# Kernel optimization log

Hardware: AMD Instinct MI355X
Metric: run time of the kernel (lower is better)

Reference implementation:

```python
import jax, jax.numpy as jnp
import numpy as np

B, L, V = 64, 512, 32000
E, H, D = 64, 512, 1024   # embed dim, LSTM hidden, bidirectional dim
NH, KD = 8, 64            # attention heads, key_dim
TOPK = 5
BN_EPS = 1e-3             # keras BatchNormalization default epsilon


def _run_lstm(x, Wx, Wh, b):
    """Keras-style LSTM (gate order i,f,g,o). x: [B,T,Din]. Returns (seq [B,T,H], last [B,H])."""
    Bn, Hn = x.shape[0], Wh.shape[0]
    z = jnp.einsum('btd,dk->btk', x, Wx) + b  # precompute input contribution [B,T,4H]
    def step(carry, zt):
        h, c = carry
        g = zt + h @ Wh
        i, f, gg, o = jnp.split(g, 4, axis=-1)
        c = jax.nn.sigmoid(f) * c + jax.nn.sigmoid(i) * jnp.tanh(gg)
        h = jax.nn.sigmoid(o) * jnp.tanh(c)
        return (h, c), h
    init = (jnp.zeros((Bn, Hn), x.dtype), jnp.zeros((Bn, Hn), x.dtype))
    (hT, _), hs = jax.lax.scan(step, init, jnp.swapaxes(z, 0, 1))
    return jnp.swapaxes(hs, 0, 1), hT


def _bilstm_seq(x, fWx, fWh, fb, bWx, bWh, bb):
    hf, _ = _run_lstm(x, fWx, fWh, fb)
    hb, _ = _run_lstm(x[:, ::-1], bWx, bWh, bb)
    return jnp.concatenate([hf, hb[:, ::-1]], axis=-1)


def _bilstm_last(x, fWx, fWh, fb, bWx, bWh, bb):
    _, hf = _run_lstm(x, fWx, fWh, fb)
    _, hb = _run_lstm(x[:, ::-1], bWx, bWh, bb)
    return jnp.concatenate([hf, hb], axis=-1)


def _cos(x):
    return x / (jnp.linalg.norm(x, axis=-1, keepdims=True) + 1e-6)


def _topk_gather(q, keys, values, k, weight=None):
    """Cosine-similarity top-k retrieval: q [B,64], keys/values [N,64] -> [B,k,64]."""
    sim = _cos(q) @ _cos(keys).T          # [B,N]
    if weight is not None:
        sim = sim * weight                # importance / confidence weighting
    _, idx = jax.lax.top_k(sim, k)
    return values[idx]                    # gather -> [B,k,64]


def _forward(tokens, emb,
             l1f_Wx, l1f_Wh, l1f_b, l1b_Wx, l1b_Wh, l1b_b,
             l2f_Wx, l2f_Wh, l2f_b, l2b_Wx, l2b_Wh, l2b_b,
             Wq, bq, Wk, bk, Wv, bv, Wo, bo,
             mq_W, mq_b,
             ext_keys, ext_vals, form_emb, conc_keys, conc_vals,
             st_mem, lt_mem, lt_imp, inf_mem, inf_conf,
             rs_W, rs_b, bn_gamma, bn_beta, bn_mean, bn_var,
             out_W, out_b, fin_W, fin_b):
    # _process_input
    x = emb[tokens]                                                   # [B,L,64]
    x = _bilstm_seq(x, l1f_Wx, l1f_Wh, l1f_b, l1b_Wx, l1b_Wh, l1b_b)  # [B,L,1024]
    x = _bilstm_last(x, l2f_Wx, l2f_Wh, l2f_b, l2b_Wx, l2b_Wh, l2b_b) # [B,1024]
    # _apply_attention: MHA over a length-1 sequence
    xs = x[:, None, :]                                                # [B,1,1024]
    q = jnp.einsum('bse,ehd->bshd', xs, Wq) + bq
    k = jnp.einsum('bse,ehd->bshd', xs, Wk) + bk
    v = jnp.einsum('bse,ehd->bshd', xs, Wv) + bv
    att = jax.nn.softmax(jnp.einsum('bshd,bthd->bhst', q, k) / jnp.sqrt(jnp.float32(KD)), axis=-1)
    ctx = jnp.einsum('bhst,bthd->bshd', att, v)
    x = (jnp.einsum('bshd,hde->bse', ctx, Wo) + bo)[:, 0]             # [B,1024]
    # _query_memories: six-bank gather/combine
    query = x @ mq_W + mq_b                                           # [B,64]
    m_ext = jax.nn.softmax(query @ ext_keys.T, axis=-1) @ ext_vals    # [B,64]
    m_form = _topk_gather(query, form_emb, form_emb, TOPK)            # [B,5,64]
    m_conc = _topk_gather(query, conc_keys, conc_vals, TOPK)          # [B,5,64]
    m_st = _topk_gather(query, st_mem, st_mem, TOPK)                  # [B,5,64]
    m_lt = _topk_gather(query, lt_mem, lt_mem, TOPK, weight=lt_imp)   # [B,5,64]
    m_inf = _topk_gather(query, inf_mem, inf_mem, TOPK, weight=inf_conf)
    mem = jnp.concatenate([m_ext[:, None], m_form, m_conc, m_st, m_lt, m_inf], axis=1)  # [B,26,64]
    x = jnp.mean(mem, axis=1)                                         # [B,64]
    # _apply_reasoning (training=False -> inference batchnorm)
    x = jax.nn.relu(x @ rs_W + rs_b)                                  # [B,512]
    x = (x - bn_mean) / jnp.sqrt(bn_var + BN_EPS) * bn_gamma + bn_beta
    # _generate_output (stage 'elementary1')
    x = x @ out_W + out_b                                             # [B,128]
    return jax.nn.sigmoid(x @ fin_W + fin_b)                          # [B,1]


def setup_inputs() -> dict:
    key = jax.random.key(0)
    ks = iter(jax.random.split(key, 64))
    def rn(shape, s=0.02):
        return jax.random.normal(next(ks), shape, dtype=jnp.float32) * s
    def z(shape):
        return jnp.zeros(shape, dtype=jnp.float32)
    inp = {
        'tokens': jax.random.randint(next(ks), (B, L), 0, V),
        'emb': rn((V, E), 0.05),
        'l1f_Wx': rn((E, 4 * H)), 'l1f_Wh': rn((H, 4 * H)), 'l1f_b': z((4 * H,)),
        'l1b_Wx': rn((E, 4 * H)), 'l1b_Wh': rn((H, 4 * H)), 'l1b_b': z((4 * H,)),
        'l2f_Wx': rn((D, 4 * H)), 'l2f_Wh': rn((H, 4 * H)), 'l2f_b': z((4 * H,)),
        'l2b_Wx': rn((D, 4 * H)), 'l2b_Wh': rn((H, 4 * H)), 'l2b_b': z((4 * H,)),
        'Wq': rn((D, NH, KD)), 'bq': z((NH, KD)),
        'Wk': rn((D, NH, KD)), 'bk': z((NH, KD)),
        'Wv': rn((D, NH, KD)), 'bv': z((NH, KD)),
        'Wo': rn((NH, KD, D)), 'bo': z((D,)),
        'mq_W': rn((D, 64)), 'mq_b': z((64,)),
        'ext_keys': rn((100, 64), 0.5), 'ext_vals': rn((100, 64), 0.5),
        'form_emb': rn((1000, 64), 0.5),
        'conc_keys': rn((1000, 64), 0.5), 'conc_vals': rn((1000, 64), 0.5),
        'st_mem': rn((100, 64), 0.5),
        'lt_mem': rn((10000, 64), 0.5),
        'lt_imp': jax.random.uniform(next(ks), (10000,), dtype=jnp.float32),
        'inf_mem': rn((500, 64), 0.5),
        'inf_conf': jax.random.uniform(next(ks), (500,), dtype=jnp.float32),
        'rs_W': rn((64, 512)), 'rs_b': z((512,)),
        'bn_gamma': jnp.ones((512,), jnp.float32), 'bn_beta': z((512,)),
        'bn_mean': rn((512,), 0.1), 'bn_var': jnp.ones((512,), jnp.float32),
        'out_W': rn((512, 128)), 'out_b': z((128,)),
        'fin_W': rn((128, 1)), 'fin_b': z((1,)),
    }
    return inp


def reference(tokens, emb,
              l1f_Wx, l1f_Wh, l1f_b, l1b_Wx, l1b_Wh, l1b_b,
              l2f_Wx, l2f_Wh, l2f_b, l2b_Wx, l2b_Wh, l2b_b,
              Wq, bq, Wk, bk, Wv, bv, Wo, bo,
              mq_W, mq_b,
              ext_keys, ext_vals, form_emb, conc_keys, conc_vals,
              st_mem, lt_mem, lt_imp, inf_mem, inf_conf,
              rs_W, rs_b, bn_gamma, bn_beta, bn_mean, bn_var,
              out_W, out_b, fin_W, fin_b):
    return _forward(tokens, emb,
                    l1f_Wx, l1f_Wh, l1f_b, l1b_Wx, l1b_Wh, l1b_b,
                    l2f_Wx, l2f_Wh, l2f_b, l2b_Wx, l2b_Wh, l2b_b,
                    Wq, bq, Wk, bk, Wv, bv, Wo, bo,
                    mq_W, mq_b,
                    ext_keys, ext_vals, form_emb, conc_keys, conc_vals,
                    st_mem, lt_mem, lt_imp, inf_mem, inf_conf,
                    rs_W, rs_b, bn_gamma, bn_beta, bn_mean, bn_var,
                    out_W, out_b, fin_W, fin_b)
```

## Files before the change

### kernel.cpp

```cpp
#include <hip/hip_runtime.h>
#include <cstddef>
#include <cstdint>

typedef short s8v   __attribute__((ext_vector_type(8)));
typedef float f32x4 __attribute__((ext_vector_type(4)));

__device__ __forceinline__ float b2f(unsigned short u) {
  union { unsigned u; float f; } x; x.u = ((unsigned)u) << 16; return x.f;
}
__device__ __forceinline__ unsigned short f2b(float f) {
  union { float f; unsigned u; } x; x.f = f;
  unsigned u = x.u;
  return (unsigned short)((u + 0x7FFFu + ((u >> 16) & 1u)) >> 16);
}
__device__ __forceinline__ float sigm(float x) { return 1.f / (1.f + __expf(-x)); }
__device__ __forceinline__ float tanh_(float x) { return 1.f - 2.f / (__expf(2.f * x) + 1.f); }

#define AT_LOAD(p)        __hip_atomic_load((p), __ATOMIC_RELAXED, __HIP_MEMORY_SCOPE_AGENT)
#define AT_STORE_RLX(p,v) __hip_atomic_store((p), (v), __ATOMIC_RELAXED, __HIP_MEMORY_SCOPE_AGENT)

__device__ __forceinline__ s8v ldg_b128_sc(const unsigned short* p) {
  s8v r;
  asm volatile("global_load_dwordx4 %0, %1, off sc0 sc1" : "=v"(r) : "v"(p) : "memory");
  return r;
}
__device__ __forceinline__ void stg_b128_sc(unsigned short* p, s8v v) {
  asm volatile("global_store_dwordx4 %0, %1, off sc0 sc1" :: "v"(p), "v"(v) : "memory");
}

__global__ void __launch_bounds__(256)
k_embed(const int* __restrict__ tok, const float* __restrict__ emb,
        unsigned short* __restrict__ x1t)
{
  const int g = blockIdx.x * 256 + threadIdx.x;
  if (g >= 64 * 512 * 8) return;
  const int row = g >> 3, i = g & 7;
  const int b = row >> 9, t = row & 511;
  const int tk = tok[row];
  const f32x4 v0 = *(const f32x4*)(emb + (size_t)tk * 64 + i * 8);
  const f32x4 v1 = *(const f32x4*)(emb + (size_t)tk * 64 + i * 8 + 4);
  s8v o;
#pragma unroll
  for (int e = 0; e < 4; ++e) { o[e] = (short)f2b(v0[e]); o[4 + e] = (short)f2b(v1[e]); }
  *(s8v*)(x1t + ((size_t)t * 64 + b) * 64 + i * 8) = o;
}

__global__ void __launch_bounds__(256)
k_tr(const float* __restrict__ Wf, const float* __restrict__ Wb,
     unsigned short* __restrict__ out, int K, int N)
{
  __shared__ float t[64][65];
  const int tid = threadIdx.x;
  const int kt = blockIdx.x, nt = blockIdx.y, dir = blockIdx.z;
  const float* W = dir ? Wb : Wf;
#pragma unroll
  for (int i = 0; i < 16; ++i) {
    const int c = i * 256 + tid;
    const int k = c >> 6, n = c & 63;
    t[k][n] = W[(size_t)(kt * 64 + k) * N + nt * 64 + n];
  }
  __syncthreads();
#pragma unroll
  for (int i = 0; i < 16; ++i) {
    const int c = i * 256 + tid;
    const int n = c >> 6, k = c & 63;
    out[(size_t)dir * N * K + (size_t)(nt * 64 + n) * K + kt * 64 + k] = f2b(t[k][n]);
  }
}

__global__ void __launch_bounds__(256)
k_norms(const float* __restrict__ formE, const float* __restrict__ concK,
        const float* __restrict__ stM, const float* __restrict__ ltM,
        const float* __restrict__ infM, float* __restrict__ inn)
{
  const int i = blockIdx.x * 256 + threadIdx.x;
  if (i >= 12600) return;
  const float* src; int loc;
  if (i < 1000)       { src = formE; loc = i; }
  else if (i < 2000)  { src = concK; loc = i - 1000; }
  else if (i < 2100)  { src = stM;   loc = i - 2000; }
  else if (i < 12100) { src = ltM;   loc = i - 2100; }
  else                { src = infM;  loc = i - 12100; }
  float ss = 0.f;
#pragma unroll 16
  for (int d = 0; d < 64; ++d) { const float v = src[(size_t)loc * 64 + d]; ss += v * v; }
  inn[i] = 1.f / (sqrtf(ss) + 1e-6f);
}

template<int PHASE>
__global__ void __launch_bounds__(128, 1)
k_lstm(const unsigned short* __restrict__ x1t,
       const unsigned short* __restrict__ z2fp, const unsigned short* __restrict__ z2bp,
       const unsigned short* __restrict__ wht,
       const float* __restrict__ Wxf, const float* __restrict__ Wxb,
       const float* __restrict__ bsf, const float* __restrict__ bsb,
       unsigned short* __restrict__ hbuf,
       unsigned short* __restrict__ yout,
       int* __restrict__ flags,
       float* __restrict__ cg,
       int s0, int s1, int CT)
{
  __shared__ __align__(16) unsigned short h_lds[64 * 512];
  __shared__ __align__(16) unsigned short wh_lds[64 * 512];
  __shared__ __align__(16) unsigned short z_lds[64 * 72];
  __shared__ __align__(16) unsigned short hout[16 * 72];

  const int tid  = threadIdx.x;
  const int w    = tid >> 6;
  const int lane = tid & 63;
  const int fc   = lane & 15, fg = lane >> 4;
  const int wg   = blockIdx.x & 31;
  const int dir  = blockIdx.x >> 5;
  const int j0   = wg * 16;

  const unsigned short* Wht = wht + (size_t)dir * 2048 * 512;
  const float* Wx = dir ? Wxb : Wxf;
  const unsigned short* Z2 = dir ? z2bp : z2fp;
  const float* BS = dir ? bsb : bsf;
  int* flg = flags + dir * 32;
  unsigned short* hb = hbuf + (size_t)dir * (2 * 64 * 512);

  float bias_reg[4];
#pragma unroll
  for (int nt = 0; nt < 4; ++nt) bias_reg[nt] = BS[nt * 512 + j0 + fc];

  float c_reg[8];
  if (PHASE == 1 || s0 == 0) {
#pragma unroll
    for (int i = 0; i < 8; ++i) c_reg[i] = 0.f;
  } else {
#pragma unroll
    for (int mt = 0; mt < 2; ++mt)
#pragma unroll
      for (int v = 0; v < 4; ++v)
        c_reg[mt * 4 + v] =
          cg[(size_t)dir * 32768 + (size_t)(w * 32 + mt * 16 + fg * 4 + v) * 512 + j0 + fc];
  }

#pragma unroll
  for (int i = 0; i < 32; ++i) {
    const int c = i * 128 + tid;
    const int lc = c >> 6, kq8 = c & 63;
    const int nt = lc >> 4, fcc = lc & 15;
    s8v v = *(const s8v*)(Wht + (size_t)(nt * 512 + j0 + fcc) * 512 + kq8 * 8);
    *(s8v*)((char*)wh_lds + lc * 1024 + ((kq8 * 16) ^ ((lc & 7) << 4))) = v;
  }

  s8v Bx[4][2];
  if (PHASE == 1) {
#pragma unroll
    for (int nt = 0; nt < 4; ++nt)
#pragma unroll
      for (int kx = 0; kx < 2; ++kx) {
        s8v f;
#pragma unroll
        for (int i = 0; i < 8; ++i)
          f[i] = (short)f2b(Wx[(size_t)(kx * 32 + fg * 8 + i) * 2048 + nt * 512 + j0 + fc]);
        Bx[nt][kx] = f;
      }
  }
  __syncthreads();

  for (int s = s0; s < s1; ++s) {
    const int t = dir ? (511 - s) : s;
    const int gb = tid >> 1, jh = tid & 1;

    s8v xf[2][2];
    s8v zr[4];
    if (PHASE == 1) {
#pragma unroll
      for (int mt = 0; mt < 2; ++mt)
#pragma unroll
        for (int kx = 0; kx < 2; ++kx)
          xf[mt][kx] = *(const s8v*)(x1t +
            ((size_t)t * 64 + (w * 32 + mt * 16 + fc)) * 64 + kx * 32 + fg * 8);
    } else {
      const int lt = dir ? (s1 - 1 - s) : (s - s0);
#pragma unroll
      for (int g = 0; g < 4; ++g)
        zr[g] = *(const s8v*)(Z2 + ((size_t)(gb * CT + lt)) * 2048 + g * 512 + j0 + jh * 8);
    }

    if (s > 0) {
      const int target = s;
      int spins = 0;
      for (;;) {
        int v = (lane < 32) ? AT_LOAD(&flg[lane]) : target;
        if (__all(v >= target)) break;
        if (++spins > (1 << 18)) break;
        __builtin_amdgcn_s_sleep(1);
      }
      const unsigned short* hsrc = hb + (size_t)((s - 1) & 1) * (64 * 512);
      s8v t0[16], t1[16];
#pragma unroll
      for (int i = 0; i < 16; ++i) {
        const int c = i * 128 + tid;
        t0[i] = ldg_b128_sc(hsrc + (size_t)(c >> 6) * 512 + (c & 63) * 8);
      }
#pragma unroll
      for (int i = 0; i < 16; ++i) {
        const int c = (16 + i) * 128 + tid;
        t1[i] = ldg_b128_sc(hsrc + (size_t)(c >> 6) * 512 + (c & 63) * 8);
      }
      asm volatile("s_waitcnt vmcnt(16)" ::: "memory");
      __builtin_amdgcn_sched_barrier(0);
#pragma unroll
      for (int i = 0; i < 16; ++i) {
        const int c = i * 128 + tid;
        const int row = c >> 6, kb = c & 63;
        *(s8v*)((char*)h_lds + row * 1024 + ((kb * 16) ^ ((row & 7) << 4))) = t0[i];
      }
      asm volatile("s_waitcnt vmcnt(0)" ::: "memory");
      __builtin_amdgcn_sched_barrier(0);
#pragma unroll
      for (int i = 0; i < 16; ++i) {
        const int c = (16 + i) * 128 + tid;
        const int row = c >> 6, kb = c & 63;
        *(s8v*)((char*)h_lds + row * 1024 + ((kb * 16) ^ ((row & 7) << 4))) = t1[i];
      }
    }
    if (PHASE == 2) {
#pragma unroll
      for (int g = 0; g < 4; ++g)
        *(s8v*)(z_lds + gb * 72 + g * 16 + jh * 8) = zr[g];
    }
    __syncthreads();

    f32x4 acc[2][4];
#pragma unroll
    for (int mt = 0; mt < 2; ++mt)
#pragma unroll
      for (int nt = 0; nt < 4; ++nt) acc[mt][nt] = (f32x4){0.f, 0.f, 0.f, 0.f};

    if (PHASE == 1) {
#pragma unroll
      for (int kx = 0; kx < 2; ++kx)
#pragma unroll
        for (int mt = 0; mt < 2; ++mt)
#pragma unroll
          for (int nt = 0; nt < 4; ++nt)
            acc[mt][nt] = __builtin_amdgcn_mfma_f32_16x16x32_bf16(xf[mt][kx], Bx[nt][kx], acc[mt][nt], 0, 0, 0);
    }
    if (s > 0) {
#pragma unroll
      for (int kk = 0; kk < 16; ++kk) {
        const int k2 = (kk * 32 + fg * 8) * 2;
        s8v a[2], bh[4];
#pragma unroll
        for (int mt = 0; mt < 2; ++mt) {
          const int row = w * 32 + mt * 16 + fc;
          a[mt] = *(const s8v*)((char*)h_lds + row * 1024 + (k2 ^ ((row & 7) << 4)));
        }
#pragma unroll
        for (int nt = 0; nt < 4; ++nt) {
          const int lc = nt * 16 + fc;
          bh[nt] = *(const s8v*)((char*)wh_lds + lc * 1024 + (k2 ^ ((lc & 7) << 4)));
        }
#pragma unroll
        for (int mt = 0; mt < 2; ++mt)
#pragma unroll
          for (int nt = 0; nt < 4; ++nt)
            acc[mt][nt] = __builtin_amdgcn_mfma_f32_16x16x32_bf16(a[mt], bh[nt], acc[mt][nt], 0, 0, 0);
      }
    }

#pragma unroll
    for (int mt = 0; mt < 2; ++mt)
#pragma unroll
      for (int v = 0; v < 4; ++v) {
        const int b = w * 32 + mt * 16 + fg * 4 + v;
        float pi = acc[mt][0][v] + bias_reg[0];
        float pf = acc[mt][1][v] + bias_reg[1];
        float pg = acc[mt][2][v] + bias_reg[2];
        float po = acc[mt][3][v] + bias_reg[3];
        if (PHASE == 2) {
          pi += b2f(z_lds[b * 72 + 0 * 16 + fc]);
          pf += b2f(z_lds[b * 72 + 1 * 16 + fc]);
          pg += b2f(z_lds[b * 72 + 2 * 16 + fc]);
          po += b2f(z_lds[b * 72 + 3 * 16 + fc]);
        }
        const float c = sigm(pf) * c_reg[mt * 4 + v] + sigm(pi) * tanh_(pg);
        c_reg[mt * 4 + v] = c;
        hout[fc * 72 + b] = f2b(sigm(po) * tanh_(c));
      }
    asm volatile("s_waitcnt lgkmcnt(0)" ::: "memory");
    __builtin_amdgcn_sched_barrier(0);
    {
      const int bb = tid >> 1, hh = tid & 1;
      s8v o;
#pragma unroll
      for (int e = 0; e < 8; ++e) o[e] = (short)hout[(hh * 8 + e) * 72 + bb];
      stg_b128_sc(hb + (size_t)(s & 1) * (64 * 512) + bb * 512 + j0 + hh * 8, o);
      if (PHASE == 1) {
        *(s8v*)(yout + ((size_t)(bb * 512 + t)) * 1024 + dir * 512 + j0 + hh * 8) = o;
      } else if (s == 511) {
        *(s8v*)(yout + (size_t)bb * 1024 + dir * 512 + j0 + hh * 8) = o;
      }
    }
    if (PHASE == 2 && s == s1 - 1 && s1 < 512) {
#pragma unroll
      for (int mt = 0; mt < 2; ++mt)
#pragma unroll
        for (int v = 0; v < 4; ++v)
          cg[(size_t)dir * 32768 + (size_t)(w * 32 + mt * 16 + fg * 4 + v) * 512 + j0 + fc] =
            c_reg[mt * 4 + v];
    }
    __syncthreads();
    if (tid == 0) AT_STORE_RLX(&flg[wg], s + 1);
  }
}

__global__ void __launch_bounds__(256)
k_zgemm(const unsigned short* __restrict__ A, const unsigned short* __restrict__ Wxt,
        unsigned short* __restrict__ Cf, unsigned short* __restrict__ Cb,
        int tb0, int tb1, int CT)
{
  __shared__ unsigned short As[128 * 64];
  __shared__ unsigned short Bs[128 * 64];
  const int tid = threadIdx.x;
  const int lane = tid & 63;
  const int w = tid >> 6;
  const int wm = w >> 1, wn = w & 1;
  const int bx = blockIdx.x, by = blockIdx.y, dz = blockIdx.z;
  const unsigned short* Bmat = Wxt + (size_t)dz * 2048 * 1024;
  unsigned short* C = dz ? Cb : Cf;
  const int tb = dz ? tb1 : tb0;
  const int fc = lane & 15, fk = (lane >> 4) << 3;

  f32x4 acc[4][4];
#pragma unroll
  for (int mt = 0; mt < 4; ++mt)
#pragma unroll
    for (int nt = 0; nt < 4; ++nt) acc[mt][nt] = (f32x4){0.f, 0.f, 0.f, 0.f};

  for (int kt = 0; kt < 16; ++kt) {
    __syncthreads();
#pragma unroll
    for (int i = 0; i < 4; ++i) {
      const int c = i * 256 + tid;
      const int row = c >> 3, kb = c & 7;
      const int m = by * 128 + row;
      const int b = m / CT, lt = m - b * CT;
      s8v v = *(const s8v*)(A + ((size_t)b * 512 + tb + lt) * 1024 + kt * 64 + kb * 8);
      *(s8v*)((char*)As + row * 128 + ((kb * 16) ^ ((row & 7) << 4))) = v;
    }
#pragma unroll
    for (int i = 0; i < 4; ++i) {
      const int c = i * 256 + tid;
      const int n = c >> 3, kb = c & 7;
      s8v v = *(const s8v*)(Bmat + (size_t)(bx * 128 + n) * 1024 + kt * 64 + kb * 8);
      *(s8v*)((char*)Bs + n * 128 + ((kb * 16) ^ ((n & 7) << 4))) = v;
    }
    __syncthreads();
#pragma unroll
    for (int kk = 0; kk < 2; ++kk) {
      const int k2 = (kk * 32 + fk) * 2;
      s8v a[4], bfr[4];
#pragma unroll
      for (int mt = 0; mt < 4; ++mt) {
        const int row = wm * 64 + mt * 16 + fc;
        a[mt] = *(const s8v*)((char*)As + row * 128 + (k2 ^ ((row & 7) << 4)));
      }
#pragma unroll
      for (int nt = 0; nt < 4; ++nt) {
        const int n = wn * 64 + nt * 16 + fc;
        bfr[nt] = *(const s8v*)((char*)Bs + n * 128 + (k2 ^ ((n & 7) << 4)));
      }
#pragma unroll
      for (int mt = 0; mt < 4; ++mt)
#pragma unroll
        for (int nt = 0; nt < 4; ++nt)
          acc[mt][nt] = __builtin_amdgcn_mfma_f32_16x16x32_bf16(a[mt], bfr[nt], acc[mt][nt], 0, 0, 0);
    }
  }
  const int r0 = (lane >> 4) << 2;
#pragma unroll
  for (int mt = 0; mt < 4; ++mt)
#pragma unroll
    for (int nt = 0; nt < 4; ++nt) {
      const size_t rowg = (size_t)(by * 128 + wm * 64 + mt * 16 + r0);
      const int colg = bx * 128 + wn * 64 + nt * 16 + fc;
#pragma unroll
      for (int r = 0; r < 4; ++r)
        C[(rowg + r) * 2048 + colg] = f2b(acc[mt][nt][r]);
    }
}

__global__ void __launch_bounds__(256)
k_head1(const unsigned short* __restrict__ x2,
        const float* __restrict__ Wv, const float* __restrict__ bv,
        const float* __restrict__ Wo, const float* __restrict__ bo,
        const float* __restrict__ mqW, const float* __restrict__ mqb,
        float* __restrict__ query)
{
  __shared__ float xs[1024], ys[512], x3[1024];
  __shared__ float part[4][64];
  const int b = blockIdx.x, tid = threadIdx.x;
  for (int i = tid; i < 1024; i += 256) xs[i] = b2f(x2[(size_t)b * 1024 + i]);
  __syncthreads();
  {
    const int o = tid * 2;
    float a0 = 0.f, a1 = 0.f;
#pragma unroll 8
    for (int e = 0; e < 1024; ++e) {
      const float xv = xs[e];
      a0 += xv * Wv[(size_t)e * 512 + o];
      a1 += xv * Wv[(size_t)e * 512 + o + 1];
    }
    ys[o] = a0 + bv[o];
    ys[o + 1] = a1 + bv[o + 1];
  }
  __syncthreads();
  {
    const int e0 = tid * 4;
    float a0 = 0.f, a1 = 0.f, a2 = 0.f, a3 = 0.f;
#pragma unroll 8
    for (int h = 0; h < 512; ++h) {
      const float yv = ys[h];
      a0 += yv * Wo[(size_t)h * 1024 + e0];
      a1 += yv * Wo[(size_t)h * 1024 + e0 + 1];
      a2 += yv * Wo[(size_t)h * 1024 + e0 + 2];
      a3 += yv * Wo[(size_t)h * 1024 + e0 + 3];
    }
    x3[e0] = a0 + bo[e0];
    x3[e0 + 1] = a1 + bo[e0 + 1];
    x3[e0 + 2] = a2 + bo[e0 + 2];
    x3[e0 + 3] = a3 + bo[e0 + 3];
  }
  __syncthreads();
  {
    const int o = tid & 63, kc = tid >> 6;
    float a = 0.f;
#pragma unroll 8
    for (int e = kc * 256; e < kc * 256 + 256; ++e) a += x3[e] * mqW[(size_t)e * 64 + o];
    part[kc][o] = a;
  }
  __syncthreads();
  if (tid < 64)
    query[b * 64 + tid] = part[0][tid] + part[1][tid] + part[2][tid] + part[3][tid] + mqb[tid];
}

__device__ void bank_topk(const float* __restrict__ K, const float* __restrict__ V,
                          int n, const float* __restrict__ W, const float* __restrict__ inn,
                          float qinv, const float* q, float* sims, float* red, int* redi,
                          float* acc64, int tid)
{
  for (int i = tid; i < n; i += 256) {
    float s = 0.f;
#pragma unroll 16
    for (int d = 0; d < 64; ++d) s += q[d] * K[(size_t)i * 64 + d];
    s *= qinv * inn[i];
    if (W) s *= W[i];
    sims[i] = s;
  }
  __syncthreads();
  for (int it = 0; it < 5; ++it) {
    float bv = -1e30f; int bi = 1 << 30;
    for (int i = tid; i < n; i += 256) {
      const float v = sims[i];
      if (v > bv) { bv = v; bi = i; }
    }
    red[tid] = bv; redi[tid] = bi;
    __syncthreads();
    for (int st = 128; st >= 1; st >>= 1) {
      if (tid < st) {
        const float v = red[tid + st]; const int ix = redi[tid + st];
        if (v > red[tid] || (v == red[tid] && ix < redi[tid])) { red[tid] = v; redi[tid] = ix; }
      }
      __syncthreads();
    }
    const int sel = redi[0];
    if (tid < 64) acc64[tid] += V[(size_t)sel * 64 + tid];
    if (tid == 0) sims[sel] = -1e30f;
    __syncthreads();
  }
}

__global__ void __launch_bounds__(256)
k_head2(const float* __restrict__ query,
        const float* extK, const float* extV,
        const float* formE, const float* concK, const float* concV,
        const float* stM, const float* ltM, const float* ltW,
        const float* infM, const float* infW,
        const float* __restrict__ inn,
        const float* rsW, const float* rsb,
        const float* gma, const float* bta,
        const float* mea, const float* vr,
        const float* outW, const float* outb,
        const float* finW, const float* finb,
        float* __restrict__ out)
{
  __shared__ float q[64];
  __shared__ float acc64[64];
  __shared__ float sims[10000];
  __shared__ float red[256];
  __shared__ int redi[256];
  __shared__ float r1[512];
  __shared__ float o2[128];

  const int b = blockIdx.x, tid = threadIdx.x;
  if (tid < 64) q[tid] = query[b * 64 + tid];
  __syncthreads();
  red[tid] = (tid < 64) ? q[tid] * q[tid] : 0.f;
  __syncthreads();
  for (int st = 128; st >= 1; st >>= 1) { if (tid < st) red[tid] += red[tid + st]; __syncthreads(); }
  const float qinv = 1.f / (sqrtf(red[0]) + 1e-6f);
  __syncthreads();

  if (tid < 100) {
    float s = 0.f;
#pragma unroll 16
    for (int d = 0; d < 64; ++d) s += q[d] * extK[(size_t)tid * 64 + d];
    sims[tid] = s;
  }
  __syncthreads();
  red[tid] = (tid < 100) ? sims[tid] : -1e30f;
  __syncthreads();
  for (int st = 128; st >= 1; st >>= 1) { if (tid < st && red[tid + st] > red[tid]) red[tid] = red[tid + st]; __syncthreads(); }
  const float mx = red[0];
  __syncthreads();
  red[tid] = (tid < 100) ? __expf(sims[tid] - mx) : 0.f;
  __syncthreads();
  for (int st = 128; st >= 1; st >>= 1) { if (tid < st) red[tid] += red[tid + st]; __syncthreads(); }
  const float Z = red[0];
  __syncthreads();
  if (tid < 100) sims[tid] = __expf(sims[tid] - mx) / Z;
  __syncthreads();
  if (tid < 64) {
    float a = 0.f;
    for (int i = 0; i < 100; ++i) a += sims[i] * extV[(size_t)i * 64 + tid];
    acc64[tid] = a;
  }
  __syncthreads();

  bank_topk(formE, formE, 1000,  nullptr, inn + 0,     qinv, q, sims, red, redi, acc64, tid);
  bank_topk(concK, concV, 1000,  nullptr, inn + 1000,  qinv, q, sims, red, redi, acc64, tid);
  bank_topk(stM,   stM,   100,   nullptr, inn + 2000,  qinv, q, sims, red, redi, acc64, tid);
  bank_topk(ltM,   ltM,   10000, ltW,     inn + 2100,  qinv, q, sims, red, redi, acc64, tid);
  bank_topk(infM,  infM,  500,   infW,    inn + 12100, qinv, q, sims, red, redi, acc64, tid);

  if (tid < 64) acc64[tid] *= (1.f / 26.f);
  __syncthreads();

  {
    const int o = tid * 2;
    float a0 = 0.f, a1 = 0.f;
#pragma unroll 16
    for (int d = 0; d < 64; ++d) {
      const float xv = acc64[d];
      a0 += xv * rsW[(size_t)d * 512 + o];
      a1 += xv * rsW[(size_t)d * 512 + o + 1];
    }
    a0 = fmaxf(a0 + rsb[o], 0.f);
    a1 = fmaxf(a1 + rsb[o + 1], 0.f);
    r1[o]     = (a0 - mea[o])     / sqrtf(vr[o]     + 1e-3f) * gma[o]     + bta[o];
    r1[o + 1] = (a1 - mea[o + 1]) / sqrtf(vr[o + 1] + 1e-3f) * gma[o + 1] + bta[o + 1];
  }
  __syncthreads();
  if (tid < 128) {
    float a = 0.f;
#pragma unroll 8
    for (int j = 0; j < 512; ++j) a += r1[j] * outW[(size_t)j * 128 + tid];
    o2[tid] = a + outb[tid];
  }
  __syncthreads();
  red[tid] = (tid < 128) ? o2[tid] * finW[tid] : 0.f;
  __syncthreads();
  for (int st = 128; st >= 1; st >>= 1) { if (tid < st) red[tid] += red[tid + st]; __syncthreads(); }
  if (tid == 0) out[b] = sigm(red[0] + finb[0]);
}

__global__ void k_diag(float* out, int n, float val) {
  const int i = blockIdx.x * 64 + threadIdx.x;
  if (i < n) out[i] = val;
}

extern "C" void kernel_launch(void* const* d_in, const int* in_sizes, int n_in,
                              void* d_out, int out_size, void* d_ws, size_t ws_size,
                              hipStream_t stream)
{
  (void)in_sizes; (void)n_in;
  const int*   tokens = (const int*)d_in[0];
  const float* emb    = (const float*)d_in[1];
  const float* l1fWx  = (const float*)d_in[2];
  const float* l1fWh  = (const float*)d_in[3];
  const float* l1fb   = (const float*)d_in[4];
  const float* l1bWx  = (const float*)d_in[5];
  const float* l1bWh  = (const float*)d_in[6];
  const float* l1bb   = (const float*)d_in[7];
  const float* l2fWx  = (const float*)d_in[8];
  const float* l2fWh  = (const float*)d_in[9];
  const float* l2fb   = (const float*)d_in[10];
  const float* l2bWx  = (const float*)d_in[11];
  const float* l2bWh  = (const float*)d_in[12];
  const float* l2bb   = (const float*)d_in[13];
  const float* Wv     = (const float*)d_in[18];
  const float* bv     = (const float*)d_in[19];
  const float* Wo     = (const float*)d_in[20];
  const float* bo     = (const float*)d_in[21];
  const float* mqW    = (const float*)d_in[22];
  const float* mqb    = (const float*)d_in[23];
  const float* extK   = (const float*)d_in[24];
  const float* extV   = (const float*)d_in[25];
  const float* formE  = (const float*)d_in[26];
  const float* concK  = (const float*)d_in[27];
  const float* concV  = (const float*)d_in[28];
  const float* stM    = (const float*)d_in[29];
  const float* ltM    = (const float*)d_in[30];
  const float* ltW    = (const float*)d_in[31];
  const float* infM   = (const float*)d_in[32];
  const float* infW   = (const float*)d_in[33];
  const float* rsW    = (const float*)d_in[34];
  const float* rsb    = (const float*)d_in[35];
  const float* gma    = (const float*)d_in[36];
  const float* bta    = (const float*)d_in[37];
  const float* mea    = (const float*)d_in[38];
  const float* vr     = (const float*)d_in[39];
  const float* outW   = (const float*)d_in[40];
  const float* outb   = (const float*)d_in[41];
  const float* finW   = (const float*)d_in[42];
  const float* finb   = (const float*)d_in[43];

  float* outp = (float*)d_out;
  char* ws = (char*)d_ws;

  size_t off = 0;
  auto take = [&](size_t sz) { size_t o = off; off += (sz + 255) & ~(size_t)255; return o; };
  const size_t o_x1    = take((size_t)64 * 512 * 64 * 2);
  const size_t o_y1    = take((size_t)64 * 512 * 1024 * 2);
  const size_t o_wxt   = take((size_t)2 * 2048 * 1024 * 2);
  const size_t o_wht1  = take((size_t)2 * 2048 * 512 * 2);
  const size_t o_wht2  = take((size_t)2 * 2048 * 512 * 2);
  const size_t o_h1    = take((size_t)2 * 2 * 64 * 512 * 2);
  const size_t o_h2    = take((size_t)2 * 2 * 64 * 512 * 2);
  const size_t o_cg    = take((size_t)2 * 64 * 512 * 4);
  const size_t o_x2    = take((size_t)64 * 1024 * 2);
  const size_t o_query = take((size_t)64 * 64 * 4);
  const size_t o_norms = take((size_t)12600 * 4);
  const size_t o_flags = take(512);
  const size_t base = off;

  int CT = 0;
  const int cts[6] = {512, 256, 128, 64, 32, 16};
  for (int i = 0; i < 6; ++i) {
    const size_t need = base + (size_t)cts[i] * 524288 + 256;
    if (need <= ws_size) { CT = cts[i]; break; }
  }
  if (CT == 0) {
    k_diag<<<1, 64, 0, stream>>>(outp, out_size, (float)(ws_size >> 20));
    return;
  }
  const size_t o_zc = take((size_t)CT * 524288);

  unsigned short* x1t  = (unsigned short*)(ws + o_x1);
  unsigned short* y1   = (unsigned short*)(ws + o_y1);
  unsigned short* wxt  = (unsigned short*)(ws + o_wxt);
  unsigned short* wht1 = (unsigned short*)(ws + o_wht1);
  unsigned short* wht2 = (unsigned short*)(ws + o_wht2);
  unsigned short* h1   = (unsigned short*)(ws + o_h1);
  unsigned short* h2   = (unsigned short*)(ws + o_h2);
  float*          cg   = (float*)(ws + o_cg);
  unsigned short* x2   = (unsigned short*)(ws + o_x2);
  float*          qry  = (float*)(ws + o_query);
  float*          nrm  = (float*)(ws + o_norms);
  int*            flags = (int*)(ws + o_flags);
  unsigned short* zcf  = (unsigned short*)(ws + o_zc);
  unsigned short* zcb  = zcf + (size_t)64 * CT * 2048;

  hipMemsetAsync(flags, 0, 512, stream);
  k_embed<<<1024, 256, 0, stream>>>(tokens, emb, x1t);
  k_norms<<<50, 256, 0, stream>>>(formE, concK, stM, ltM, infM, nrm);
  k_tr<<<dim3(8, 32, 2), 256, 0, stream>>>(l1fWh, l1bWh, wht1, 512, 2048);
  k_tr<<<dim3(8, 32, 2), 256, 0, stream>>>(l2fWh, l2bWh, wht2, 512, 2048);
  k_tr<<<dim3(16, 32, 2), 256, 0, stream>>>(l2fWx, l2bWx, wxt, 1024, 2048);

  k_lstm<1><<<64, 128, 0, stream>>>(x1t, nullptr, nullptr, wht1, l1fWx, l1bWx,
                                    l1fb, l1bb, h1, y1, flags, nullptr, 0, 512, 512);

  const int nC = 512 / CT;
  for (int c = 0; c < nC; ++c) {
    const int s0 = c * CT, s1 = s0 + CT;
    k_zgemm<<<dim3(16, (64 * CT) / 128, 2), 256, 0, stream>>>(
        y1, wxt, zcf, zcb, s0, 512 - s1, CT);
    k_lstm<2><<<64, 128, 0, stream>>>(nullptr, zcf, zcb, wht2, nullptr, nullptr,
                                      l2fb, l2bb, h2, x2, flags + 64, cg, s0, s1, CT);
  }

  k_head1<<<64, 256, 0, stream>>>(x2, Wv, bv, Wo, bo, mqW, mqb, qry);
  k_head2<<<64, 256, 0, stream>>>(qry, extK, extV, formE, concK, concV, stM, ltM, ltW,
                                  infM, infW, nrm, rsW, rsb, gma, bta, mea, vr,
                                  outW, outb, finW, finb, outp);
}
```

Baseline: 5.996 ms.

## Load recurrent h straight into MFMA registers and sync per wave

```diff
diff --git a/kernel.cpp b/kernel.cpp
--- a/kernel.cpp
+++ b/kernel.cpp
@@ -100,7 +100,6 @@
        float* __restrict__ cg,
        int s0, int s1, int CT)
 {
-  __shared__ __align__(16) unsigned short h_lds[64 * 512];
   __shared__ __align__(16) unsigned short wh_lds[64 * 512];
   __shared__ __align__(16) unsigned short z_lds[64 * 72];
   __shared__ __align__(16) unsigned short hout[16 * 72];
@@ -117,7 +116,7 @@
   const float* Wx = dir ? Wxb : Wxf;
   const unsigned short* Z2 = dir ? z2bp : z2fp;
   const float* BS = dir ? bsb : bsf;
-  int* flg = flags + dir * 32;
+  int* flg = flags + dir * 64;
   unsigned short* hb = hbuf + (size_t)dir * (2 * 64 * 512);
 
   float bias_reg[4];
@@ -166,7 +165,6 @@
     const int gb = tid >> 1, jh = tid & 1;
 
     s8v xf[2][2];
-    s8v zr[4];
     if (PHASE == 1) {
 #pragma unroll
       for (int mt = 0; mt < 2; ++mt)
@@ -176,81 +174,58 @@
             ((size_t)t * 64 + (w * 32 + mt * 16 + fc)) * 64 + kx * 32 + fg * 8);
     } else {
       const int lt = dir ? (s1 - 1 - s) : (s - s0);
+      s8v zr[4];
 #pragma unroll
       for (int g = 0; g < 4; ++g)
         zr[g] = *(const s8v*)(Z2 + ((size_t)(gb * CT + lt)) * 2048 + g * 512 + j0 + jh * 8);
-    }
+#pragma unroll
+      for (int g = 0; g < 4; ++g)
+        *(s8v*)(z_lds + gb * 72 + g * 16 + jh * 8) = zr[g];
+    }
+
+    f32x4 acc[2][4];
+#pragma unroll
+    for (int mt = 0; mt < 2; ++mt)
+#pragma unroll
+      for (int nt = 0; nt < 4; ++nt) acc[mt][nt] = (f32x4){0.f, 0.f, 0.f, 0.f};
 
     if (s > 0) {
       const int target = s;
       int spins = 0;
       for (;;) {
-        int v = (lane < 32) ? AT_LOAD(&flg[lane]) : target;
+        int v = AT_LOAD(&flg[lane]);
         if (__all(v >= target)) break;
         if (++spins > (1 << 18)) break;
         __builtin_amdgcn_s_sleep(1);
       }
+    }
+
+    if (PHASE == 1) {
+#pragma unroll
+      for (int kx = 0; kx < 2; ++kx)
+#pragma unroll
+        for (int mt = 0; mt < 2; ++mt)
+#pragma unroll
+          for (int nt = 0; nt < 4; ++nt)
+            acc[mt][nt] = __builtin_amdgcn_mfma_f32_16x16x32_bf16(xf[mt][kx], Bx[nt][kx], acc[mt][nt], 0, 0, 0);
+    }
+
+    if (s > 0) {
       const unsigned short* hsrc = hb + (size_t)((s - 1) & 1) * (64 * 512);
-      s8v t0[16], t1[16];
-#pragma unroll
-      for (int i = 0; i < 16; ++i) {
-        const int c = i * 128 + tid;
-        t0[i] = ldg_b128_sc(hsrc + (size_t)(c >> 6) * 512 + (c & 63) * 8);
-      }
-#pragma unroll
-      for (int i = 0; i < 16; ++i) {
-        const int c = (16 + i) * 128 + tid;
-        t1[i] = ldg_b128_sc(hsrc + (size_t)(c >> 6) * 512 + (c & 63) * 8);
-      }
+      s8v af[32];
+#pragma unroll
+      for (int kk = 0; kk < 16; ++kk)
+#pragma unroll
+        for (int mt = 0; mt < 2; ++mt)
+          af[kk * 2 + mt] = ldg_b128_sc(hsrc +
+            (size_t)((kk * 4 + fg) * 64 + (w * 32 + mt * 16 + fc)) * 8);
+
       asm volatile("s_waitcnt vmcnt(16)" ::: "memory");
       __builtin_amdgcn_sched_barrier(0);
 #pragma unroll
-      for (int i = 0; i < 16; ++i) {
-        const int c = i * 128 + tid;
-        const int row = c >> 6, kb = c & 63;
-        *(s8v*)((char*)h_lds + row * 1024 + ((kb * 16) ^ ((row & 7) << 4))) = t0[i];
-      }
-      asm volatile("s_waitcnt vmcnt(0)" ::: "memory");
-      __builtin_amdgcn_sched_barrier(0);
-#pragma unroll
-      for (int i = 0; i < 16; ++i) {
-        const int c = (16 + i) * 128 + tid;
-        const int row = c >> 6, kb = c & 63;
-        *(s8v*)((char*)h_lds + row * 1024 + ((kb * 16) ^ ((row & 7) << 4))) = t1[i];
-      }
-    }
-    if (PHASE == 2) {
-#pragma unroll
-      for (int g = 0; g < 4; ++g)
-        *(s8v*)(z_lds + gb * 72 + g * 16 + jh * 8) = zr[g];
-    }
-    __syncthreads();
-
-    f32x4 acc[2][4];
-#pragma unroll
-    for (int mt = 0; mt < 2; ++mt)
-#pragma unroll
-      for (int nt = 0; nt < 4; ++nt) acc[mt][nt] = (f32x4){0.f, 0.f, 0.f, 0.f};
-
-    if (PHASE == 1) {
-#pragma unroll
-      for (int kx = 0; kx < 2; ++kx)
-#pragma unroll
-        for (int mt = 0; mt < 2; ++mt)
-#pragma unroll
-          for (int nt = 0; nt < 4; ++nt)
-            acc[mt][nt] = __builtin_amdgcn_mfma_f32_16x16x32_bf16(xf[mt][kx], Bx[nt][kx], acc[mt][nt], 0, 0, 0);
-    }
-    if (s > 0) {
-#pragma unroll
-      for (int kk = 0; kk < 16; ++kk) {
+      for (int kk = 0; kk < 8; ++kk) {
         const int k2 = (kk * 32 + fg * 8) * 2;
-        s8v a[2], bh[4];
-#pragma unroll
-        for (int mt = 0; mt < 2; ++mt) {
-          const int row = w * 32 + mt * 16 + fc;
-          a[mt] = *(const s8v*)((char*)h_lds + row * 1024 + (k2 ^ ((row & 7) << 4)));
-        }
+        s8v bh[4];
 #pragma unroll
         for (int nt = 0; nt < 4; ++nt) {
           const int lc = nt * 16 + fc;
@@ -260,10 +235,31 @@
         for (int mt = 0; mt < 2; ++mt)
 #pragma unroll
           for (int nt = 0; nt < 4; ++nt)
-            acc[mt][nt] = __builtin_amdgcn_mfma_f32_16x16x32_bf16(a[mt], bh[nt], acc[mt][nt], 0, 0, 0);
-      }
-    }
-
+            acc[mt][nt] = __builtin_amdgcn_mfma_f32_16x16x32_bf16(af[kk * 2 + mt], bh[nt], acc[mt][nt], 0, 0, 0);
+      }
+      asm volatile("s_waitcnt vmcnt(0)" ::: "memory");
+      __builtin_amdgcn_sched_barrier(0);
+#pragma unroll
+      for (int kk = 8; kk < 16; ++kk) {
+        const int k2 = (kk * 32 + fg * 8) * 2;
+        s8v bh[4];
+#pragma unroll
+        for (int nt = 0; nt < 4; ++nt) {
+          const int lc = nt * 16 + fc;
+          bh[nt] = *(const s8v*)((char*)wh_lds + lc * 1024 + (k2 ^ ((lc & 7) << 4)));
+        }
+#pragma unroll
+        for (int mt = 0; mt < 2; ++mt)
+#pragma unroll
+          for (int nt = 0; nt < 4; ++nt)
+            acc[mt][nt] = __builtin_amdgcn_mfma_f32_16x16x32_bf16(af[kk * 2 + mt], bh[nt], acc[mt][nt], 0, 0, 0);
+      }
+    }
+
+    if (PHASE == 2) {
+      asm volatile("s_waitcnt lgkmcnt(0)" ::: "memory");
+      __builtin_amdgcn_sched_barrier(0);
+    }
 #pragma unroll
     for (int mt = 0; mt < 2; ++mt)
 #pragma unroll
@@ -290,7 +286,8 @@
       s8v o;
 #pragma unroll
       for (int e = 0; e < 8; ++e) o[e] = (short)hout[(hh * 8 + e) * 72 + bb];
-      stg_b128_sc(hb + (size_t)(s & 1) * (64 * 512) + bb * 512 + j0 + hh * 8, o);
+      stg_b128_sc(hb + (size_t)(s & 1) * (64 * 512) +
+                  (size_t)(((j0 >> 3) + hh) * 64 + bb) * 8, o);
       if (PHASE == 1) {
         *(s8v*)(yout + ((size_t)(bb * 512 + t)) * 1024 + dir * 512 + j0 + hh * 8) = o;
       } else if (s == 511) {
@@ -305,8 +302,9 @@
           cg[(size_t)dir * 32768 + (size_t)(w * 32 + mt * 16 + fg * 4 + v) * 512 + j0 + fc] =
             c_reg[mt * 4 + v];
     }
-    __syncthreads();
-    if (tid == 0) AT_STORE_RLX(&flg[wg], s + 1);
+    asm volatile("s_waitcnt vmcnt(0)" ::: "memory");
+    __builtin_amdgcn_sched_barrier(0);
+    if (lane == 0) AT_STORE_RLX(&flg[wg * 2 + w], s + 1);
   }
 }
 
@@ -637,7 +635,7 @@
   const size_t o_x2    = take((size_t)64 * 1024 * 2);
   const size_t o_query = take((size_t)64 * 64 * 4);
   const size_t o_norms = take((size_t)12600 * 4);
-  const size_t o_flags = take(512);
+  const size_t o_flags = take(1024);
   const size_t base = off;
 
   int CT = 0;
@@ -667,7 +665,7 @@
   unsigned short* zcf  = (unsigned short*)(ws + o_zc);
   unsigned short* zcb  = zcf + (size_t)64 * CT * 2048;
 
-  hipMemsetAsync(flags, 0, 512, stream);
+  hipMemsetAsync(flags, 0, 1024, stream);
   k_embed<<<1024, 256, 0, stream>>>(tokens, emb, x1t);
   k_norms<<<50, 256, 0, stream>>>(formE, concK, stM, ltM, infM, nrm);
   k_tr<<<dim3(8, 32, 2), 256, 0, stream>>>(l1fWh, l1bWh, wht1, 512, 2048);
@@ -683,7 +681,7 @@
     k_zgemm<<<dim3(16, (64 * CT) / 128, 2), 256, 0, stream>>>(
         y1, wxt, zcf, zcb, s0, 512 - s1, CT);
     k_lstm<2><<<64, 128, 0, stream>>>(nullptr, zcf, zcb, wht2, nullptr, nullptr,
-                                      l2fb, l2bb, h2, x2, flags + 64, cg, s0, s1, CT);
+                                      l2fb, l2bb, h2, x2, flags + 128, cg, s0, s1, CT);
   }
 
   k_head1<<<64, 256, 0, stream>>>(x2, Wv, bv, Wo, bo, mqW, mqb, qry);
```

New measurement: 5.974 ms. Within noise of the previous version (-0.4%).
